# Performance work log

Hardware: AMD Instinct MI355X
Metric: run time of the kernel (lower is better)

Reference implementation:

```python
import jax, jax.numpy as jnp
import numpy as np

MAX_SPAN_WIDTH = 30
NUM_WORDS = 2048
NUM_CAND = 8192
HIDDEN = 768
FEAT = 20
FFNN = 1000
SPAN_DIM = HIDDEN * 3 + FEAT  # 2324
TOP_SPAN_NUM = int(NUM_WORDS * 0.4)  # 819


def setup_inputs() -> dict:
    key = jax.random.key(0)
    ks = jax.random.split(key, 16)
    mention_doc = jax.random.normal(ks[0], (NUM_WORDS, HIDDEN), jnp.float32)
    starts = jax.random.randint(ks[1], (NUM_CAND,), 0, NUM_WORDS - MAX_SPAN_WIDTH, jnp.int32)
    widths = jax.random.randint(ks[2], (NUM_CAND,), 1, MAX_SPAN_WIDTH + 1, jnp.int32)
    ends = jnp.minimum(starts + widths - 1, NUM_WORDS - 1).astype(jnp.int32)
    s = 0.02
    lin = lambda k, i, o: jax.random.normal(k, (i, o), jnp.float32) * s
    return dict(
        mention_doc=mention_doc,
        span_width_emb=jax.random.normal(ks[3], (MAX_SPAN_WIDTH, FEAT), jnp.float32) * s,
        head_w=jax.random.normal(ks[4], (HIDDEN,), jnp.float32) * s,
        head_b=jnp.zeros((), jnp.float32),
        m_w1=lin(ks[5], SPAN_DIM, FFNN), m_b1=jnp.zeros((FFNN,), jnp.float32),
        m_w2=lin(ks[6], FFNN, FFNN), m_b2=jnp.zeros((FFNN,), jnp.float32),
        m_w3=jax.random.normal(ks[7], (FFNN,), jnp.float32) * s, m_b3=jnp.zeros((), jnp.float32),
        width_prior_emb=jax.random.normal(ks[8], (MAX_SPAN_WIDTH, FEAT), jnp.float32) * s,
        w_w1=lin(ks[9], FEAT, FFNN), w_b1=jnp.zeros((FFNN,), jnp.float32),
        w_w2=lin(ks[10], FFNN, FFNN), w_b2=jnp.zeros((FFNN,), jnp.float32),
        w_w3=jax.random.normal(ks[11], (FFNN,), jnp.float32) * s, w_b3=jnp.zeros((), jnp.float32),
        candidate_starts=starts,
        candidate_ends=ends,
        top_span_num=TOP_SPAN_NUM,
    )


def get_span_emb(mention_doc, starts, ends, span_width_emb, head_w, head_b):
    # mention_doc: [N, H]; starts/ends: [C]
    num_words = mention_doc.shape[0]
    start_emb = mention_doc[starts]              # [C, H]
    end_emb = mention_doc[ends]                  # [C, H]
    width_ids = ends - starts                    # span width - 1, in [0, MAX_SPAN_WIDTH)
    width_emb = span_width_emb[width_ids]        # [C, F]
    offs = jnp.arange(MAX_SPAN_WIDTH, dtype=starts.dtype)
    idxes = jnp.minimum(starts[:, None] + offs[None, :], num_words - 1)  # [C, W]
    emb_spans = mention_doc[idxes]               # [C, W, H]  (dominant intermediate)
    head_scores = mention_doc @ head_w + head_b  # [N]
    hs = head_scores[idxes]                      # [C, W]
    mask = offs[None, :] <= width_ids[:, None]
    hs = jnp.where(mask, hs, -jnp.inf)
    attn = jax.nn.softmax(hs, axis=1)            # masked softmax over span positions
    attended = jnp.einsum('cw,cwh->ch', attn, emb_spans)
    return jnp.concatenate([start_emb, end_emb, width_emb, attended], axis=-1)  # [C, 3H+F]


def ffnn3(x, w1, b1, w2, b2, w3, b3):
    h = jax.nn.relu(x @ w1 + b1)
    h = jax.nn.relu(h @ w2 + b2)
    return h @ w3 + b3  # [..., ] scalar score per row (Squeezer)


def extract_top_spans(span_scores, starts, ends, top_span_num, num_words):
    # Greedy crossing-interval NMS, faithful to the original sequential algorithm.
    C = span_scores.shape[0]
    order = jnp.argsort(-span_scores)
    offs = jnp.arange(MAX_SPAN_WIDTH, dtype=jnp.int32)

    def body(i, state):
        max_end, min_start, sel, count = state
        idx = order[i]
        s = starts[idx]
        e = ends[idx]
        dup = max_end[s] == e
        j_raw = s + offs
        j = jnp.minimum(j_raw, num_words - 1)
        in_span = j_raw <= e
        # crossing: an already-selected span starting at j>s ends beyond e,
        # or one ending at j<e starts before s.
        c1 = in_span & (j_raw > s) & (max_end[j] > e)
        c2 = in_span & (j_raw < e) & (min_start[j] < s)
        crossed = jnp.any(c1 | c2)
        accept = (~dup) & (~crossed) & (count < top_span_num)
        sel = jnp.where(accept, sel.at[count].set(idx.astype(jnp.int32)), sel)
        max_end = jnp.where(accept, max_end.at[s].max(e), max_end)
        min_start = jnp.where(accept, min_start.at[e].min(s), min_start)
        count = count + accept.astype(jnp.int32)
        return (max_end, min_start, sel, count)

    max_end0 = jnp.full((num_words,), -1, jnp.int32)          # 'not set' sentinel
    min_start0 = jnp.full((num_words,), num_words, jnp.int32)  # 'not set' sentinel
    sel0 = jnp.zeros((top_span_num,), jnp.int32)
    _, _, sel, count = jax.lax.fori_loop(0, C, body, (max_end0, min_start0, sel0, jnp.int32(0)))

    # sort selected spans by (start, end); pad unfilled slots with the first sorted span
    valid = jnp.arange(top_span_num) < count
    keys = jnp.where(valid, starts[sel] * num_words + ends[sel], jnp.iinfo(jnp.int32).max)
    sorted_sel = sel[jnp.argsort(keys)]
    return jnp.where(valid, sorted_sel, sorted_sel[0])


def reference(mention_doc, span_width_emb, head_w, head_b,
              m_w1, m_b1, m_w2, m_b2, m_w3, m_b3,
              width_prior_emb, w_w1, w_b1, w_w2, w_b2, w_w3, w_b3,
              candidate_starts, candidate_ends, top_span_num):
    num_words = mention_doc.shape[0]
    span_emb = get_span_emb(mention_doc, candidate_starts, candidate_ends,
                            span_width_emb, head_w, head_b)            # [C, 2324]
    mention_scores = ffnn3(span_emb, m_w1, m_b1, m_w2, m_b2, m_w3, m_b3)  # [C]
    width_scores = ffnn3(width_prior_emb, w_w1, w_b1, w_w2, w_b2, w_w3, w_b3)  # [30]
    cand_mention_scores = mention_scores + width_scores[candidate_ends - candidate_starts]
    top_idx = extract_top_spans(cand_mention_scores, candidate_starts, candidate_ends,
                                top_span_num, num_words)               # [top]
    top_starts = candidate_starts[top_idx]
    top_ends = candidate_ends[top_idx]
    top_span_emb = span_emb[top_idx]
    top_scores = cand_mention_scores[top_idx]
    return (cand_mention_scores, top_idx, top_starts, top_ends, top_span_emb, top_scores)
```

## Files before the change

### kernel.cpp

```cpp
#include <hip/hip_runtime.h>
#include <cstdio>
#include <cmath>

#define NUM_WORDS 2048
#define NUM_CAND 8192
#define HIDDEN 768
#define FEAT 20
#define FFNN_DIM 1000
#define SPAN_DIM 2324
#define TOP_NUM 819
#define MSW 30
#define KP2 1024
#define NP 1024
#define PNP 3072

#define OUT_TOPIDX   (NUM_CAND)
#define OUT_TSTART   (NUM_CAND + TOP_NUM)
#define OUT_TEND     (NUM_CAND + 2*TOP_NUM)
#define OUT_TEMB     (NUM_CAND + 3*TOP_NUM)
#define OUT_TSCORE   (NUM_CAND + 3*TOP_NUM + TOP_NUM*SPAN_DIM)

typedef short short8 __attribute__((ext_vector_type(8)));
typedef float f32x4 __attribute__((ext_vector_type(4)));
typedef unsigned short u16x4 __attribute__((ext_vector_type(4)));

__device__ __forceinline__ unsigned short bf16_rne(float x) {
    unsigned int u = __float_as_uint(x);
    unsigned int r = u + 0x7FFFu + ((u >> 16) & 1u);
    return (unsigned short)(r >> 16);
}
__device__ __forceinline__ float bf16_to_f(unsigned short h) {
    return __uint_as_float(((unsigned int)h) << 16);
}
__device__ __forceinline__ void store_split2(unsigned short* p0, unsigned short* p1,
                                             size_t off, float v) {
    unsigned short h0 = bf16_rne(v);
    float r1 = v - bf16_to_f(h0);
    p0[off] = h0;
    p1[off] = bf16_rne(r1);
}

__device__ __forceinline__ void gl_lds16(const unsigned short* g, unsigned short* l) {
    __builtin_amdgcn_global_load_lds(
        (const __attribute__((address_space(1))) unsigned short*)g,
        (__attribute__((address_space(3))) unsigned short*)l, 16, 0, 0);
}

__global__ void head_kernel(const float* __restrict__ doc, const float* __restrict__ hw,
                            const float* __restrict__ hb, float* __restrict__ out,
                            int* __restrict__ hist,
                            unsigned short* __restrict__ d0, unsigned short* __restrict__ d1) {
    int t = threadIdx.x;
    if (blockIdx.x == 0) {
        for (int i = t; i < NUM_WORDS; i += 256) hist[i] = 0;
    }
    int base = blockIdx.x * 4 * HIDDEN;
    for (int i = t; i < 4 * HIDDEN; i += 256)
        store_split2(d0, d1, (size_t)base + i, doc[base + i]);
    int wave = t >> 6, lane = t & 63;
    int row = blockIdx.x * 4 + wave;
    if (row >= NUM_WORDS) return;
    float acc = 0.f;
    for (int h = lane; h < HIDDEN; h += 64) acc += doc[row * HIDDEN + h] * hw[h];
    for (int off = 32; off > 0; off >>= 1) acc += __shfl_down(acc, off);
    if (lane == 0) out[row] = acc + hb[0];
}

__global__ void width_kernel(const float* __restrict__ x, const float* __restrict__ w1,
                             const float* __restrict__ b1, const float* __restrict__ w2,
                             const float* __restrict__ b2, const float* __restrict__ w3,
                             const float* __restrict__ b3, float* __restrict__ out,
                             const float* __restrict__ swe, const float* __restrict__ mw1,
                             float* __restrict__ tw) {
    __shared__ float xs[FEAT];
    __shared__ float h1s[FFNN_DIM];
    __shared__ float red[256];
    int r = blockIdx.x, t = threadIdx.x;
    if (t < FEAT) xs[t] = x[r * FEAT + t];
    __syncthreads();
    for (int j = t; j < FFNN_DIM; j += 256) {
        float acc = b1[j];
        for (int k = 0; k < FEAT; ++k) acc += xs[k] * w1[k * FFNN_DIM + j];
        h1s[j] = fmaxf(acc, 0.f);
    }
    __syncthreads();
    float partial = 0.f;
    for (int j = t; j < FFNN_DIM; j += 256) {
        float acc = b2[j];
        for (int k = 0; k < FFNN_DIM; ++k) acc += h1s[k] * w2[k * FFNN_DIM + j];
        partial += fmaxf(acc, 0.f) * w3[j];
    }
    red[t] = partial;
    __syncthreads();
    for (int s = 128; s > 0; s >>= 1) { if (t < s) red[t] += red[t + s]; __syncthreads(); }
    if (t == 0) out[r] = red[0] + b3[0];
    for (int n = t; n < NP; n += 256) {
        float acc = 0.f;
        if (n < FFNN_DIM) {
            for (int f = 0; f < FEAT; ++f)
                acc += swe[r * FEAT + f] * mw1[(size_t)(1536 + f) * FFNN_DIM + n];
        }
        tw[r * NP + n] = acc;
    }
}

__global__ void attn_kernel(const float* __restrict__ head_s, const int* __restrict__ starts,
                            const int* __restrict__ ends, float* __restrict__ attn_g,
                            int* __restrict__ hist) {
    int wave = threadIdx.x >> 6, w = threadIdx.x & 63;
    int c = blockIdx.x * 4 + wave;
    if (c >= NUM_CAND) return;
    int s = starts[c], e = ends[c];
    if (w == 0) atomicAdd(&hist[s], 1);
    int wid = e - s;
    float hsv = -INFINITY;
    if (w < MSW && w <= wid) hsv = head_s[s + w];
    float m = hsv;
    for (int off = 32; off > 0; off >>= 1) m = fmaxf(m, __shfl_down(m, off));
    m = __shfl(m, 0);
    float ex = (w < MSW && w <= wid) ? expf(hsv - m) : 0.f;
    float ssum = ex;
    for (int off = 32; off > 0; off >>= 1) ssum += __shfl_down(ssum, off);
    ssum = __shfl(ssum, 0);
    if (w < 32) attn_g[c * 32 + w] = (w < MSW) ? (ex / ssum) : 0.f;
}

__global__ __launch_bounds__(256) void perm_kernel(const int* __restrict__ hist,
                                                   const int* __restrict__ starts,
                                                   int* __restrict__ perm) {
    __shared__ int hoff[NUM_WORDS];
    __shared__ int wsum[4];
    int t = threadIdx.x, lane = t & 63, wv = t >> 6;
    int base = t * 8;
    int lh[8];
    int s0 = 0;
#pragma unroll
    for (int i = 0; i < 8; ++i) { lh[i] = hist[base + i]; s0 += lh[i]; }
    int sc = s0;
    for (int o = 1; o < 64; o <<= 1) { int v = __shfl_up(sc, o); if (lane >= o) sc += v; }
    if (lane == 63) wsum[wv] = sc;
    __syncthreads();
    int wbase = 0;
    for (int i = 0; i < wv; ++i) wbase += wsum[i];
    int run = wbase + sc - s0;
#pragma unroll
    for (int i = 0; i < 8; ++i) { hoff[base + i] = run; run += lh[i]; }
    __syncthreads();
    for (int c = t; c < NUM_CAND; c += 256) {
        int pos = atomicAdd(&hoff[starts[c]], 1);
        perm[pos] = c;
    }
}

__global__ __launch_bounds__(256) void convert_wc(const float* __restrict__ w1,
                                                  unsigned short* __restrict__ q0,
                                                  unsigned short* __restrict__ q1) {
    __shared__ float tile[64][65];
    int kbase = blockIdx.x << 6;
    int n2base = blockIdx.y << 6;
    int seg = n2base >> 10;
    int nbase = n2base & 1023;
    int row0 = (seg == 0) ? 0 : ((seg == 1) ? HIDDEN : 1556);
    int t = threadIdx.x;
    int c = t & 63, r0 = t >> 6;
    for (int rr = 0; rr < 64; rr += 4) {
        int r = rr + r0;
        int n = nbase + c;
        tile[r][c] = (n < FFNN_DIM) ? w1[(size_t)(row0 + kbase + r) * FFNN_DIM + n] : 0.f;
    }
    __syncthreads();
    int kl = t & 63;
    for (int rr = 0; rr < 64; rr += 4) {
        int nl = rr + r0;
        store_split2(q0, q1, (size_t)(n2base + nl) * HIDDEN + kbase + kl, tile[kl][nl]);
    }
}

__global__ __launch_bounds__(256) void convert_wt(const float* __restrict__ w,
                                                  unsigned short* __restrict__ q0,
                                                  unsigned short* __restrict__ q1) {
    __shared__ float tile[64][65];
    int kbase = blockIdx.x << 6;
    int nbase = blockIdx.y << 6;
    int t = threadIdx.x;
    int c = t & 63, r0 = t >> 6;
    for (int rr = 0; rr < 64; rr += 4) {
        int r = rr + r0;
        int k = kbase + r, n = nbase + c;
        tile[r][c] = (k < FFNN_DIM && n < FFNN_DIM) ? w[(size_t)k * FFNN_DIM + n] : 0.f;
    }
    __syncthreads();
    int kl = t & 63;
    for (int rr = 0; rr < 64; rr += 4) {
        int nl = rr + r0;
        store_split2(q0, q1, (size_t)(nbase + nl) * KP2 + kbase + kl, tile[kl][nl]);
    }
}

__device__ __forceinline__ void stage_tile(const unsigned short* __restrict__ src,
                                           unsigned short* lds, int base_row, int Kp, int k0,
                                           int t) {
#pragma unroll
    for (int qi = 0; qi < 2; ++qi) {
        int u = qi * 256 + t;
        int l = u & 63;
        int row = ((u >> 6) << 4) + (l >> 2);
        int cblk = (l & 3) ^ (row & 3);
        const unsigned short* g = src + (size_t)(base_row + row) * Kp + k0 + cblk * 8;
        gl_lds16(g, lds + u * 8);
    }
}

__global__ __launch_bounds__(256, 2) void gemm3p(
    const unsigned short* __restrict__ A0, const unsigned short* __restrict__ A1,
    const unsigned short* __restrict__ B0, const unsigned short* __restrict__ B1,
    float* __restrict__ C) {
    __shared__ unsigned short As0[128 * 32], As1[128 * 32];
    __shared__ unsigned short Bs0[128 * 32], Bs1[128 * 32];
    int t = threadIdx.x;
    int bid = blockIdx.x;
    int bm = (bid & 15) << 7;
    int bn = (bid >> 4) << 7;
    int lane = t & 63, wv = t >> 6;
    int wm = (wv >> 1) * 64, wn = (wv & 1) * 64;
    int lr = lane & 15, qq = lane >> 4;
    int sw = (qq ^ (lr & 3)) * 8;

    f32x4 acc[4][4] = {};

    for (int k0 = 0; k0 < HIDDEN; k0 += 32) {
        stage_tile(A0, As0, bm, HIDDEN, k0, t);
        stage_tile(A1, As1, bm, HIDDEN, k0, t);
        stage_tile(B0, Bs0, bn, HIDDEN, k0, t);
        stage_tile(B1, Bs1, bn, HIDDEN, k0, t);
        __syncthreads();
        short8 a0[4], a1[4];
#pragma unroll
        for (int i = 0; i < 4; ++i) {
            int ra = (wm + i * 16 + lr) * 32 + sw;
            a0[i] = *(const short8*)&As0[ra];
            a1[i] = *(const short8*)&As1[ra];
        }
#pragma unroll
        for (int j = 0; j < 4; ++j) {
            int rb = (wn + j * 16 + lr) * 32 + sw;
            short8 b0 = *(const short8*)&Bs0[rb];
            short8 b1 = *(const short8*)&Bs1[rb];
#pragma unroll
            for (int i = 0; i < 4; ++i) {
                acc[i][j] = __builtin_amdgcn_mfma_f32_16x16x32_bf16(a1[i], b0, acc[i][j], 0, 0, 0);
                acc[i][j] = __builtin_amdgcn_mfma_f32_16x16x32_bf16(a0[i], b1, acc[i][j], 0, 0, 0);
                acc[i][j] = __builtin_amdgcn_mfma_f32_16x16x32_bf16(a0[i], b0, acc[i][j], 0, 0, 0);
            }
        }
        __syncthreads();
    }
#pragma unroll
    for (int i = 0; i < 4; ++i)
#pragma unroll
        for (int j = 0; j < 4; ++j)
#pragma unroll
            for (int r = 0; r < 4; ++r) {
                int m = bm + wm + i * 16 + qq * 4 + r;
                int n = bn + wn + j * 16 + lr;
                C[(size_t)m * PNP + n] = acc[i][j][r];
            }
}

__global__ void combine_kernel(const float* __restrict__ P, const float* __restrict__ tw,
                               const float* __restrict__ attn_g, const float* __restrict__ b1,
                               const int* __restrict__ starts, const int* __restrict__ ends,
                               const int* __restrict__ perm,
                               unsigned short* __restrict__ h0, unsigned short* __restrict__ h1) {
    int pos = ((blockIdx.x & 7) << 10) | (blockIdx.x >> 3);
    int c = perm[pos];
    int t = threadIdx.x;
    int s = starts[c], e = ends[c];
    int wid = e - s;
    __shared__ float at[MSW];
    if (t < MSW) at[t] = attn_g[c * 32 + t];
    __syncthreads();
    int n0 = t * 4;
    size_t ho = (size_t)c * NP + n0;
    if (t < 250) {
        f32x4 acc = *(const f32x4*)&P[(size_t)s * PNP + n0];
        acc += *(const f32x4*)&P[(size_t)e * PNP + 1024 + n0];
        acc += *(const f32x4*)&tw[(size_t)wid * NP + n0];
        acc += *(const f32x4*)&b1[n0];
        const float* Pa = P + (size_t)s * PNP + 2048 + n0;
        for (int w = 0; w <= wid; ++w)
            acc += at[w] * *(const f32x4*)&Pa[(size_t)w * PNP];
        u16x4 q0, q1;
#pragma unroll
        for (int k = 0; k < 4; ++k) {
            float v = fmaxf(acc[k], 0.f);
            unsigned short x0 = bf16_rne(v);
            float r1 = v - bf16_to_f(x0);
            q0[k] = x0; q1[k] = bf16_rne(r1);
        }
        *(u16x4*)&h0[ho] = q0;
        *(u16x4*)&h1[ho] = q1;
    } else {
        u16x4 z = {0, 0, 0, 0};
        *(u16x4*)&h0[ho] = z;
        *(u16x4*)&h1[ho] = z;
    }
}

__global__ __launch_bounds__(256, 2) void gemm3(
    const unsigned short* __restrict__ A0, const unsigned short* __restrict__ A1,
    const unsigned short* __restrict__ B0, const unsigned short* __restrict__ B1,
    const float* __restrict__ bias, int nreal, int Kp,
    const float* __restrict__ w3, float* __restrict__ partials) {
    __shared__ unsigned short As0[128 * 32], As1[128 * 32];
    __shared__ unsigned short Bs0[128 * 32], Bs1[128 * 32];
    int t = threadIdx.x;
    int bid = blockIdx.x;
    int sm = bid >> 6, idx = bid & 63;
    int bm = ((sm << 3) + (idx & 7)) << 7;
    int bn = (idx >> 3) << 7;
    int lane = t & 63, wv = t >> 6;
    int wm = (wv >> 1) * 64, wn = (wv & 1) * 64;
    int lr = lane & 15, qq = lane >> 4;
    int sw = (qq ^ (lr & 3)) * 8;

    f32x4 acc[4][4] = {};

    for (int k0 = 0; k0 < Kp; k0 += 32) {
        stage_tile(A0, As0, bm, Kp, k0, t);
        stage_tile(A1, As1, bm, Kp, k0, t);
        stage_tile(B0, Bs0, bn, Kp, k0, t);
        stage_tile(B1, Bs1, bn, Kp, k0, t);
        __syncthreads();
        short8 a0[4], a1[4];
#pragma unroll
        for (int i = 0; i < 4; ++i) {
            int ra = (wm + i * 16 + lr) * 32 + sw;
            a0[i] = *(const short8*)&As0[ra];
            a1[i] = *(const short8*)&As1[ra];
        }
#pragma unroll
        for (int j = 0; j < 4; ++j) {
            int rb = (wn + j * 16 + lr) * 32 + sw;
            short8 b0 = *(const short8*)&Bs0[rb];
            short8 b1 = *(const short8*)&Bs1[rb];
#pragma unroll
            for (int i = 0; i < 4; ++i) {
                acc[i][j] = __builtin_amdgcn_mfma_f32_16x16x32_bf16(a1[i], b0, acc[i][j], 0, 0, 0);
                acc[i][j] = __builtin_amdgcn_mfma_f32_16x16x32_bf16(a0[i], b1, acc[i][j], 0, 0, 0);
                acc[i][j] = __builtin_amdgcn_mfma_f32_16x16x32_bf16(a0[i], b0, acc[i][j], 0, 0, 0);
            }
        }
        __syncthreads();
    }

    int pid = ((bn >> 7) << 1) | (wn >> 6);
#pragma unroll
    for (int i = 0; i < 4; ++i)
#pragma unroll
        for (int r = 0; r < 4; ++r) {
            float p = 0.f;
#pragma unroll
            for (int j = 0; j < 4; ++j) {
                int n = bn + wn + j * 16 + lr;
                float v = acc[i][j][r] + (n < nreal ? bias[n] : 0.f);
                v = fmaxf(v, 0.f);
                p += v * (n < nreal ? w3[n] : 0.f);
            }
            p += __shfl_xor(p, 1);
            p += __shfl_xor(p, 2);
            p += __shfl_xor(p, 4);
            p += __shfl_xor(p, 8);
            if (lr == 0) {
                int m = bm + wm + i * 16 + qq * 4 + r;
                partials[(size_t)m * 16 + pid] = p;
            }
        }
}

__global__ void score_final(const float* __restrict__ partials, const float* __restrict__ b3,
                            const float* __restrict__ width_s, const int* __restrict__ starts,
                            const int* __restrict__ ends, float* __restrict__ out) {
    int c = blockIdx.x * 256 + threadIdx.x;
    if (c >= NUM_CAND) return;
    float s = b3[0] + width_s[ends[c] - starts[c]];
#pragma unroll
    for (int p = 0; p < 16; ++p) s += partials[(size_t)c * 16 + p];
    out[c] = s;
}

__global__ __launch_bounds__(256) void rank_kernel(const float* __restrict__ scores,
                                                   const int* __restrict__ starts,
                                                   const int* __restrict__ ends,
                                                   unsigned short* __restrict__ ord_g,
                                                   unsigned int* __restrict__ se_g) {
    __shared__ unsigned long long kk[NUM_CAND];
    int t = threadIdx.x;
    for (int i = t; i < NUM_CAND; i += 256) {
        unsigned int b = __float_as_uint(scores[i]);
        unsigned int u = b ^ ((b & 0x80000000u) ? 0xFFFFFFFFu : 0x80000000u);
        unsigned int hi = ~u;
        kk[i] = ((unsigned long long)hi << 32) | (unsigned int)i;
    }
    __syncthreads();
    int c = blockIdx.x * 32 + (t >> 3);
    int seg = (t & 7) * 1024;
    unsigned long long mykey = kk[c];
    int cnt = 0;
    for (int i = seg; i < seg + 1024; ++i) cnt += (kk[i] < mykey) ? 1 : 0;
    cnt += __shfl_xor(cnt, 1);
    cnt += __shfl_xor(cnt, 2);
    cnt += __shfl_xor(cnt, 4);
    if ((t & 7) == 0) {
        int idx = (int)(mykey & 0xFFFFFFFFull);
        int rank = cnt;
        ord_g[rank] = (unsigned short)idx;
        se_g[rank] = ((unsigned int)starts[idx] << 16) | (unsigned int)ends[idx];
    }
}

__global__ __launch_bounds__(64, 1)
void select_nms(const unsigned int* __restrict__ se_g,
                unsigned short* __restrict__ sel_g,
                int* __restrict__ count_g) {
    __shared__ unsigned int se_arr[NUM_CAND];
    __shared__ unsigned int st[2 * NUM_WORDS];
    int lane = threadIdx.x;

    {
        const uint4* src4 = (const uint4*)se_g;
        uint4* dst4 = (uint4*)se_arr;
        for (int i = lane; i < NUM_CAND / 4; i += 64) dst4[i] = src4[i];
    }
    for (int i = lane; i < 2 * NUM_WORDS; i += 64)
        st[i] = (i & 1) ? (unsigned int)NUM_WORDS : 0u;
    __syncthreads();

    const unsigned long long* stp = (const unsigned long long*)st;
    int count = 0;
    for (int c = 0; c < NUM_CAND / 64; ++c) {
        int ib = c * 64;
        unsigned int sev = se_arr[ib + lane];
        int s = (int)(sev >> 16), e = (int)(sev & 0xFFFFu);
        const unsigned long long* bp = stp + s;
        unsigned long long v[MSW];
#pragma unroll
        for (int w = 0; w < MSW; ++w) v[w] = bp[w];
        int me = (int)(unsigned int)v[0] - 1;
        bool crossedA = (s < e) && ((int)(unsigned int)(v[0] >> 32) < s);
        bool crossedB = false;
#pragma unroll
        for (int w = 1; w < MSW; ++w) {
            int j = s + w;
            bool in = (j <= e);
            int mej = (int)(unsigned int)v[w] - 1;
            int msj = (int)(unsigned int)(v[w] >> 32);
            bool hit = in && ((mej > e) || ((j < e) && (msj < s)));
            if (w & 1) crossedA = crossedA || hit;
            else       crossedB = crossedB || hit;
        }
        bool crossed = crossedA || crossedB;
        bool spec = !crossed && (me != e);

        int cbefore = count;
        unsigned long long window = ~0ull;
        unsigned int pend = 0u;
        int rk = 0, lcnt = 0;
        while (true) {
            unsigned long long b = __ballot(spec) & window;
            if (b == 0ull) break;
            int f = __ffsll((unsigned long long)b) - 1;
            unsigned int sef = __builtin_amdgcn_readlane(sev, (unsigned int)f);
            int sf = (int)(sef >> 16), ef = (int)(sef & 0xFFFFu);
            bool mine = (lane == lcnt);
            pend = mine ? sef : pend;
            rk = mine ? (ib + f) : rk;
            lcnt++;
            count++;
            if (count >= TOP_NUM) break;
            window &= (f >= 63) ? 0ull : (~0ull << (f + 1));
            if (lane > f) {
                if (s == sf) me = max(me, ef);
                crossed = crossed || ((s < sf) && (sf <= e) && (ef > e))
                                  || ((sf < s) && (s <= ef) && (ef < e));
                spec = !crossed && (me != e);
            }
        }
        if (lane < lcnt) {
            int sf = (int)(pend >> 16), ef = (int)(pend & 0xFFFFu);
            sel_g[cbefore + lane] = (unsigned short)rk;
            atomicMax(&st[2 * sf], (unsigned int)(ef + 1));
            atomicMin(&st[2 * ef + 1], (unsigned int)sf);
        }
        if (count >= TOP_NUM) break;
    }
    if (lane == 0) *count_g = count;
}

__global__ __launch_bounds__(1024) void select_post(const float* __restrict__ scores,
                                                    const int* __restrict__ starts,
                                                    const int* __restrict__ ends,
                                                    const unsigned short* __restrict__ ord_g,
                                                    const unsigned short* __restrict__ sel_g,
                                                    const int* __restrict__ count_g,
                                                    float* out, int* top_idx_ws) {
    __shared__ unsigned long long fkeys[1024];
    int t = threadIdx.x;
    int count = *count_g;
    {
        unsigned long long k = 0xFFFFFFFFFFFFFFFFull;
        if (t < count) {
            int idx = (int)ord_g[sel_g[t]];
            unsigned int key32 = (unsigned int)(starts[idx] * NUM_WORDS + ends[idx]);
            k = ((unsigned long long)key32 << 32) | (unsigned int)idx;
        }
        fkeys[t] = k;
    }
    __syncthreads();
    for (int size = 2; size <= 1024; size <<= 1) {
        for (int stride = size >> 1; stride > 0; stride >>= 1) {
            int ixj = t ^ stride;
            if (ixj > t) {
                bool up = ((t & size) == 0);
                unsigned long long a = fkeys[t], b = fkeys[ixj];
                if ((a > b) == up) { fkeys[t] = b; fkeys[ixj] = a; }
            }
            __syncthreads();
        }
    }
    if (t < TOP_NUM) {
        int fi = (t < count) ? (int)(fkeys[t] & 0xFFFFFFFFull)
                             : (int)(fkeys[0] & 0xFFFFFFFFull);
        out[OUT_TOPIDX + t] = (float)fi;
        out[OUT_TSTART + t] = (float)starts[fi];
        out[OUT_TEND + t] = (float)ends[fi];
        out[OUT_TSCORE + t] = scores[fi];
        top_idx_ws[t] = fi;
    }
}

__global__ void gather_emb(const float* __restrict__ doc, const float* __restrict__ swe,
                           const float* __restrict__ attn_g, const int* __restrict__ starts,
                           const int* __restrict__ ends, const int* __restrict__ top_idx_ws,
                           float* __restrict__ out) {
    int r = blockIdx.x, t = threadIdx.x;
    int idx = top_idx_ws[r];
    int s = starts[idx], e = ends[idx];
    int wid = e - s;
    __shared__ float at[MSW];
    if (t < MSW) at[t] = attn_g[(size_t)idx * 32 + t];
    __syncthreads();
    float* dst = out + OUT_TEMB + (size_t)r * SPAN_DIM;
    if (t < 192) {
        int h4 = t * 4;
        f32x4 vs = *(const f32x4*)&doc[(size_t)s * HIDDEN + h4];
        f32x4 ve = *(const f32x4*)&doc[(size_t)e * HIDDEN + h4];
        f32x4 acc = {0.f, 0.f, 0.f, 0.f};
        for (int w = 0; w <= wid; ++w)
            acc += at[w] * *(const f32x4*)&doc[(size_t)(s + w) * HIDDEN + h4];
#pragma unroll
        for (int k = 0; k < 4; ++k) {
            dst[h4 + k] = vs[k];
            dst[HIDDEN + h4 + k] = ve[k];
            dst[2 * HIDDEN + FEAT + h4 + k] = acc[k];
        }
    }
    if (t < FEAT) dst[2 * HIDDEN + t] = swe[wid * FEAT + t];
}

extern "C" void kernel_launch(void* const* d_in, const int* in_sizes, int n_in,
                              void* d_out, int out_size, void* d_ws, size_t ws_size,
                              hipStream_t stream) {
    const float* mention_doc = (const float*)d_in[0];
    const float* span_width_emb = (const float*)d_in[1];
    const float* head_w = (const float*)d_in[2];
    const float* head_b = (const float*)d_in[3];
    const float* m_w1 = (const float*)d_in[4];
    const float* m_b1 = (const float*)d_in[5];
    const float* m_w2 = (const float*)d_in[6];
    const float* m_b2 = (const float*)d_in[7];
    const float* m_w3 = (const float*)d_in[8];
    const float* m_b3 = (const float*)d_in[9];
    const float* width_prior_emb = (const float*)d_in[10];
    const float* w_w1 = (const float*)d_in[11];
    const float* w_b1 = (const float*)d_in[12];
    const float* w_w2 = (const float*)d_in[13];
    const float* w_b2 = (const float*)d_in[14];
    const float* w_w3 = (const float*)d_in[15];
    const float* w_b3 = (const float*)d_in[16];
    const int* cand_starts = (const int*)d_in[17];
    const int* cand_ends = (const int*)d_in[18];

    char* w = (char*)d_ws;
    const size_t szH = (size_t)NUM_CAND * NP * 2;
    const size_t szW2 = (size_t)NP * KP2 * 2;
    const size_t szWc = (size_t)PNP * HIDDEN * 2;
    const size_t szD = (size_t)NUM_WORDS * HIDDEN * 2;
    char* p = w;
    unsigned short* h0 = (unsigned short*)p; p += szH;
    unsigned short* h1 = (unsigned short*)p; p += szH;
    unsigned short* w2t0 = (unsigned short*)p; p += szW2;
    unsigned short* w2t1 = (unsigned short*)p; p += szW2;
    unsigned short* Wc0 = (unsigned short*)p; p += szWc;
    unsigned short* Wc1 = (unsigned short*)p; p += szWc;
    unsigned short* d0 = (unsigned short*)p; p += szD;
    unsigned short* d1 = (unsigned short*)p; p += szD;
    float* P = (float*)p; p += (size_t)NUM_WORDS * PNP * 4;
    float* tw = (float*)p; p += (size_t)MSW * NP * 4;
    float* attn_g = (float*)p; p += (size_t)NUM_CAND * 32 * 4;
    float* partials = (float*)p; p += (size_t)NUM_CAND * 16 * 4;
    unsigned short* ord_g = (unsigned short*)p; p += (size_t)NUM_CAND * 2;
    unsigned int* se_g = (unsigned int*)p; p += (size_t)NUM_CAND * 4;
    unsigned short* sel_g = (unsigned short*)p; p += 2048;
    int* count_g = (int*)p; p += 128;
    float* head_s = (float*)p; p += NUM_WORDS * 4;
    float* width_s = (float*)p; p += 128;
    int* top_idx_ws = (int*)p; p += 4096;
    int* hist_g = (int*)p; p += NUM_WORDS * 4;
    int* perm_g = (int*)p; p += (size_t)NUM_CAND * 4;

    size_t need = (size_t)(p - w);
    if (ws_size < need) {
        fprintf(stderr, "kernel_launch: ws too small (%zu < %zu)\n", ws_size, need);
    }

    float* out = (float*)d_out;

    head_kernel<<<NUM_WORDS / 4, 256, 0, stream>>>(mention_doc, head_w, head_b, head_s,
                                                   hist_g, d0, d1);
    width_kernel<<<MSW, 256, 0, stream>>>(width_prior_emb, w_w1, w_b1, w_w2, w_b2, w_w3, w_b3,
                                          width_s, span_width_emb, m_w1, tw);
    attn_kernel<<<NUM_CAND / 4, 256, 0, stream>>>(head_s, cand_starts, cand_ends, attn_g,
                                                  hist_g);
    convert_wc<<<dim3(12, 48), 256, 0, stream>>>(m_w1, Wc0, Wc1);
    convert_wt<<<dim3(16, 16), 256, 0, stream>>>(m_w2, w2t0, w2t1);
    perm_kernel<<<1, 256, 0, stream>>>(hist_g, cand_starts, perm_g);
    gemm3p<<<16 * 24, 256, 0, stream>>>(d0, d1, Wc0, Wc1, P);
    combine_kernel<<<NUM_CAND, 256, 0, stream>>>(P, tw, attn_g, m_b1, cand_starts, cand_ends,
                                                 perm_g, h0, h1);
    gemm3<<<512, 256, 0, stream>>>(h0, h1, w2t0, w2t1, m_b2, FFNN_DIM, KP2,
                                   m_w3, partials);
    score_final<<<NUM_CAND / 256, 256, 0, stream>>>(partials, m_b3, width_s, cand_starts,
                                                    cand_ends, out);
    rank_kernel<<<NUM_CAND / 32, 256, 0, stream>>>(out, cand_starts, cand_ends, ord_g, se_g);
    select_nms<<<1, 64, 0, stream>>>(se_g, sel_g, count_g);
    select_post<<<1, 1024, 0, stream>>>(out, cand_starts, cand_ends, ord_g, sel_g, count_g,
                                        out, top_idx_ws);
    gather_emb<<<TOP_NUM, 256, 0, stream>>>(mention_doc, span_width_emb, attn_g, cand_starts,
                                            cand_ends, top_idx_ws, out);
}
```

Measured before the change: 766.6 us.

## Double GEMM K-tile to 64 with 8-way LDS swizzle, remap blocks, rotate rank scan

Both split-bf16 GEMM kernels now stage 64-wide K slices per iteration instead of 32, using an 8-slot XOR swizzle, which halves the number of barriers and loop iterations. Block-to-tile mapping is changed in both GEMMs, grouping blocks for better L2 locality. The rank kernel rotates each thread's scan start within its segment to reduce LDS bank conflicts. The trade-off is doubled LDS use (64KB per block), which may limit occupancy to fewer than two blocks per CU.

Measured after the change: 746.8 us. 2.6% less time.

```diff
diff --git a/kernel.cpp b/kernel.cpp
--- a/kernel.cpp
+++ b/kernel.cpp
@@ -197,16 +197,16 @@
     }
 }
 
-__device__ __forceinline__ void stage_tile(const unsigned short* __restrict__ src,
-                                           unsigned short* lds, int base_row, int Kp, int k0,
-                                           int t) {
-#pragma unroll
-    for (int qi = 0; qi < 2; ++qi) {
+__device__ __forceinline__ void stage_tile64(const unsigned short* __restrict__ src,
+                                             unsigned short* lds, int base_row, int Kp,
+                                             int k0, int t) {
+#pragma unroll
+    for (int qi = 0; qi < 4; ++qi) {
         int u = qi * 256 + t;
-        int l = u & 63;
-        int row = ((u >> 6) << 4) + (l >> 2);
-        int cblk = (l & 3) ^ (row & 3);
-        const unsigned short* g = src + (size_t)(base_row + row) * Kp + k0 + cblk * 8;
+        int row = u >> 3;
+        int slot = u & 7;
+        int kblk = slot ^ (row & 7);
+        const unsigned short* g = src + (size_t)(base_row + row) * Kp + k0 + kblk * 8;
         gl_lds16(g, lds + u * 8);
     }
 }
@@ -215,42 +215,54 @@
     const unsigned short* __restrict__ A0, const unsigned short* __restrict__ A1,
     const unsigned short* __restrict__ B0, const unsigned short* __restrict__ B1,
     float* __restrict__ C) {
-    __shared__ unsigned short As0[128 * 32], As1[128 * 32];
-    __shared__ unsigned short Bs0[128 * 32], Bs1[128 * 32];
+    __shared__ unsigned short As0[128 * 64], As1[128 * 64];
+    __shared__ unsigned short Bs0[128 * 64], Bs1[128 * 64];
     int t = threadIdx.x;
     int bid = blockIdx.x;
-    int bm = (bid & 15) << 7;
-    int bn = (bid >> 4) << 7;
+    int g = bid & 7, rr = bid >> 3;
+    int bm = (rr & 15) << 7;
+    int bn = (g + 8 * (rr >> 4)) << 7;
     int lane = t & 63, wv = t >> 6;
     int wm = (wv >> 1) * 64, wn = (wv & 1) * 64;
     int lr = lane & 15, qq = lane >> 4;
-    int sw = (qq ^ (lr & 3)) * 8;
 
     f32x4 acc[4][4] = {};
 
-    for (int k0 = 0; k0 < HIDDEN; k0 += 32) {
-        stage_tile(A0, As0, bm, HIDDEN, k0, t);
-        stage_tile(A1, As1, bm, HIDDEN, k0, t);
-        stage_tile(B0, Bs0, bn, HIDDEN, k0, t);
-        stage_tile(B1, Bs1, bn, HIDDEN, k0, t);
+    for (int k0 = 0; k0 < HIDDEN; k0 += 64) {
+        stage_tile64(A0, As0, bm, HIDDEN, k0, t);
+        stage_tile64(A1, As1, bm, HIDDEN, k0, t);
+        stage_tile64(B0, Bs0, bn, HIDDEN, k0, t);
+        stage_tile64(B1, Bs1, bn, HIDDEN, k0, t);
         __syncthreads();
-        short8 a0[4], a1[4];
+        short8 a0[2][4], a1[2][4];
 #pragma unroll
         for (int i = 0; i < 4; ++i) {
-            int ra = (wm + i * 16 + lr) * 32 + sw;
-            a0[i] = *(const short8*)&As0[ra];
-            a1[i] = *(const short8*)&As1[ra];
+            int ra = (wm + i * 16 + lr) * 64;
+#pragma unroll
+            for (int h = 0; h < 2; ++h) {
+                int sl = ((h * 4 + qq) ^ (lr & 7)) * 8;
+                a0[h][i] = *(const short8*)&As0[ra + sl];
+                a1[h][i] = *(const short8*)&As1[ra + sl];
+            }
         }
 #pragma unroll
         for (int j = 0; j < 4; ++j) {
-            int rb = (wn + j * 16 + lr) * 32 + sw;
-            short8 b0 = *(const short8*)&Bs0[rb];
-            short8 b1 = *(const short8*)&Bs1[rb];
+            int rb = (wn + j * 16 + lr) * 64;
+            short8 b0[2], b1[2];
+#pragma unroll
+            for (int h = 0; h < 2; ++h) {
+                int sl = ((h * 4 + qq) ^ (lr & 7)) * 8;
+                b0[h] = *(const short8*)&Bs0[rb + sl];
+                b1[h] = *(const short8*)&Bs1[rb + sl];
+            }
 #pragma unroll
             for (int i = 0; i < 4; ++i) {
-                acc[i][j] = __builtin_amdgcn_mfma_f32_16x16x32_bf16(a1[i], b0, acc[i][j], 0, 0, 0);
-                acc[i][j] = __builtin_amdgcn_mfma_f32_16x16x32_bf16(a0[i], b1, acc[i][j], 0, 0, 0);
-                acc[i][j] = __builtin_amdgcn_mfma_f32_16x16x32_bf16(a0[i], b0, acc[i][j], 0, 0, 0);
+#pragma unroll
+                for (int h = 0; h < 2; ++h) {
+                    acc[i][j] = __builtin_amdgcn_mfma_f32_16x16x32_bf16(a1[h][i], b0[h], acc[i][j], 0, 0, 0);
+                    acc[i][j] = __builtin_amdgcn_mfma_f32_16x16x32_bf16(a0[h][i], b1[h], acc[i][j], 0, 0, 0);
+                    acc[i][j] = __builtin_amdgcn_mfma_f32_16x16x32_bf16(a0[h][i], b0[h], acc[i][j], 0, 0, 0);
+                }
             }
         }
         __syncthreads();
@@ -312,43 +324,53 @@
     const unsigned short* __restrict__ B0, const unsigned short* __restrict__ B1,
     const float* __restrict__ bias, int nreal, int Kp,
     const float* __restrict__ w3, float* __restrict__ partials) {
-    __shared__ unsigned short As0[128 * 32], As1[128 * 32];
-    __shared__ unsigned short Bs0[128 * 32], Bs1[128 * 32];
+    __shared__ unsigned short As0[128 * 64], As1[128 * 64];
+    __shared__ unsigned short Bs0[128 * 64], Bs1[128 * 64];
     int t = threadIdx.x;
     int bid = blockIdx.x;
-    int sm = bid >> 6, idx = bid & 63;
-    int bm = ((sm << 3) + (idx & 7)) << 7;
-    int bn = (idx >> 3) << 7;
+    int bm = (bid >> 3) << 7;
+    int bn = (bid & 7) << 7;
     int lane = t & 63, wv = t >> 6;
     int wm = (wv >> 1) * 64, wn = (wv & 1) * 64;
     int lr = lane & 15, qq = lane >> 4;
-    int sw = (qq ^ (lr & 3)) * 8;
 
     f32x4 acc[4][4] = {};
 
-    for (int k0 = 0; k0 < Kp; k0 += 32) {
-        stage_tile(A0, As0, bm, Kp, k0, t);
-        stage_tile(A1, As1, bm, Kp, k0, t);
-        stage_tile(B0, Bs0, bn, Kp, k0, t);
-        stage_tile(B1, Bs1, bn, Kp, k0, t);
+    for (int k0 = 0; k0 < Kp; k0 += 64) {
+        stage_tile64(A0, As0, bm, Kp, k0, t);
+        stage_tile64(A1, As1, bm, Kp, k0, t);
+        stage_tile64(B0, Bs0, bn, Kp, k0, t);
+        stage_tile64(B1, Bs1, bn, Kp, k0, t);
         __syncthreads();
-        short8 a0[4], a1[4];
+        short8 a0[2][4], a1[2][4];
 #pragma unroll
         for (int i = 0; i < 4; ++i) {
-            int ra = (wm + i * 16 + lr) * 32 + sw;
-            a0[i] = *(const short8*)&As0[ra];
-            a1[i] = *(const short8*)&As1[ra];
+            int ra = (wm + i * 16 + lr) * 64;
+#pragma unroll
+            for (int h = 0; h < 2; ++h) {
+                int sl = ((h * 4 + qq) ^ (lr & 7)) * 8;
+                a0[h][i] = *(const short8*)&As0[ra + sl];
+                a1[h][i] = *(const short8*)&As1[ra + sl];
+            }
         }
 #pragma unroll
         for (int j = 0; j < 4; ++j) {
-            int rb = (wn + j * 16 + lr) * 32 + sw;
-            short8 b0 = *(const short8*)&Bs0[rb];
-            short8 b1 = *(const short8*)&Bs1[rb];
+            int rb = (wn + j * 16 + lr) * 64;
+            short8 b0[2], b1[2];
+#pragma unroll
+            for (int h = 0; h < 2; ++h) {
+                int sl = ((h * 4 + qq) ^ (lr & 7)) * 8;
+                b0[h] = *(const short8*)&Bs0[rb + sl];
+                b1[h] = *(const short8*)&Bs1[rb + sl];
+            }
 #pragma unroll
             for (int i = 0; i < 4; ++i) {
-                acc[i][j] = __builtin_amdgcn_mfma_f32_16x16x32_bf16(a1[i], b0, acc[i][j], 0, 0, 0);
-                acc[i][j] = __builtin_amdgcn_mfma_f32_16x16x32_bf16(a0[i], b1, acc[i][j], 0, 0, 0);
-                acc[i][j] = __builtin_amdgcn_mfma_f32_16x16x32_bf16(a0[i], b0, acc[i][j], 0, 0, 0);
+#pragma unroll
+                for (int h = 0; h < 2; ++h) {
+                    acc[i][j] = __builtin_amdgcn_mfma_f32_16x16x32_bf16(a1[h][i], b0[h], acc[i][j], 0, 0, 0);
+                    acc[i][j] = __builtin_amdgcn_mfma_f32_16x16x32_bf16(a0[h][i], b1[h], acc[i][j], 0, 0, 0);
+                    acc[i][j] = __builtin_amdgcn_mfma_f32_16x16x32_bf16(a0[h][i], b0[h], acc[i][j], 0, 0, 0);
+                }
             }
         }
         __syncthreads();
@@ -405,9 +427,13 @@
     __syncthreads();
     int c = blockIdx.x * 32 + (t >> 3);
     int seg = (t & 7) * 1024;
+    int rot = (t & 7) * 2;
     unsigned long long mykey = kk[c];
     int cnt = 0;
-    for (int i = seg; i < seg + 1024; ++i) cnt += (kk[i] < mykey) ? 1 : 0;
+    for (int ii = 0; ii < 1024; ++ii) {
+        int i = seg + ((ii + rot) & 1023);
+        cnt += (kk[i] < mykey) ? 1 : 0;
+    }
     cnt += __shfl_xor(cnt, 1);
     cnt += __shfl_xor(cnt, 2);
     cnt += __shfl_xor(cnt, 4);
```
